# Kernel optimization log

Hardware: AMD Instinct MI355X
Metric: run time of the kernel (lower is better)

Reference implementation:

```python
import jax, jax.numpy as jnp
import numpy as np

B, IN, H, OUT = 4096, 1024, 2048, 1024
EPS = 1e-5  # added to std (not variance), matching the torch module


def _ln(z, a, b):
    # torch.std default is unbiased (ddof=1); eps added to sigma
    mu = jnp.mean(z, axis=1, keepdims=True)
    sigma = jnp.std(z, axis=1, ddof=1, keepdims=True)
    return (z - mu) / (sigma + EPS) * a + b


def setup_inputs() -> dict:
    key = jax.random.key(0)
    ks = iter(jax.random.split(key, 40))
    W = lambda i, o: (jax.random.normal(next(ks), (o, i), jnp.float32) / np.sqrt(i)).astype(jnp.float32)
    bz = lambda o: jnp.zeros((o,), jnp.float32)
    d = {
        "inp": jax.random.normal(next(ks), (B, IN), jnp.float32),
        "h_0": jax.random.normal(next(ks), (B, H), jnp.float32),
        "c_0": jax.random.normal(next(ks), (B, H), jnp.float32),
        # h-side gate linears (H -> H)
        "Wfh": W(H, H), "bfh": bz(H), "Wih": W(H, H), "bih": bz(H),
        "Wch": W(H, H), "bch": bz(H), "Woh": W(H, H), "boh": bz(H),
        # x-side gate linears (IN -> H)
        "Wfx": W(IN, H), "bfx": bz(H), "Wix": W(IN, H), "bix": bz(H),
        "Wcx": W(IN, H), "bcx": bz(H), "Wox": W(IN, H), "box": bz(H),
        # decoder (H -> OUT)
        "Wdec": W(H, OUT), "bdec": bz(OUT),
        # LayerNormalization params (a2 ones, b2 zeros), shape (1, H)
        "ax": jnp.ones((1, H), jnp.float32), "bx": jnp.zeros((1, H), jnp.float32),
        "ah": jnp.ones((1, H), jnp.float32), "bh": jnp.zeros((1, H), jnp.float32),
        "ac": jnp.ones((1, H), jnp.float32), "bc": jnp.zeros((1, H), jnp.float32),
    }
    return d


def reference(inp, h_0, c_0,
              Wfh, bfh, Wih, bih, Wch, bch, Woh, boh,
              Wfx, bfx, Wix, bix, Wcx, bcx, Wox, box,
              Wdec, bdec, ax, bx, ah, bh, ac, bc):
    lin = lambda x, W, b: x @ W.T + b
    gate = lambda wx, bx_, wh, bh_: (_ln(lin(inp, wx, bx_), ax, bx)
                                     + _ln(lin(h_0, wh, bh_), ah, bh))
    f_g = jax.nn.sigmoid(gate(Wfx, bfx, Wfh, bfh))
    i_g = jax.nn.sigmoid(gate(Wix, bix, Wih, bih))
    c_tilda = jnp.tanh(gate(Wcx, bcx, Wch, bch))
    cx = f_g * c_0 + i_g * c_tilda
    o_g = jax.nn.sigmoid(gate(Wox, box, Woh, boh))
    hx = o_g * jnp.tanh(_ln(cx, ac, bc))
    out = lin(hx, Wdec, bdec)  # decoder applied to hidden state (vectorized over batch)
    return (out, hx, cx)
```

## Files before the change

### kernel.cpp

```cpp
#include <hip/hip_runtime.h>

#define NB   4096
#define NIN  1024
#define NH   2048
#define NOUT 1024
#define NH4  8192

typedef short short8 __attribute__((ext_vector_type(8)));
typedef float f32x4 __attribute__((ext_vector_type(4)));
typedef float f32x16 __attribute__((ext_vector_type(16)));
typedef unsigned short ushort8v __attribute__((ext_vector_type(8)));

__device__ __forceinline__ float bf2f(unsigned short u) {
  union { unsigned int i; float f; } c; c.i = ((unsigned int)u) << 16; return c.f;
}
__device__ __forceinline__ unsigned short f2bf(float f) {
  union { float f; unsigned int i; } c; c.f = f;
  unsigned int u = c.i;
  u += 0x7FFFu + ((u >> 16) & 1u);
  return (unsigned short)(u >> 16);
}
__device__ __forceinline__ float sigf(float x) { return 1.0f / (1.0f + __expf(-x)); }
__device__ __forceinline__ float tanh_f(float x) { return 1.0f - 2.0f / (__expf(2.0f * x) + 1.0f); }

#define CNT_INP  ((size_t)NB * NIN)
#define CNT_H0   ((size_t)NB * NH)
#define CNT_WXG  ((size_t)NH * NIN)
#define CNT_WHG  ((size_t)NH * NH)
#define CNT_WD   ((size_t)NOUT * NH)
#define OFF_XB   ((size_t)0)
#define OFF_H0B  (OFF_XB + CNT_INP)
#define OFF_HXB  (OFF_H0B + CNT_H0)
#define OFF_WX   (OFF_HXB + CNT_H0)
#define OFF_WH   (OFF_WX + 4 * CNT_WXG)
#define OFF_WD   (OFF_WH + 4 * CNT_WHG)
#define OFF_ZX   (OFF_WD + CNT_WD)
#define OFF_ZH   (OFF_ZX + (size_t)NB * NH4)
#define CVT_TOTAL (OFF_WD + CNT_WD)

struct CvtArgs { const float* src[11]; };

__global__ __launch_bounds__(256) void cvt_all(CvtArgs a, unsigned short* __restrict__ dstBase) {
  const size_t i = ((size_t)blockIdx.x * 256 + threadIdx.x) * 8;
  if (i >= CVT_TOTAL) return;
  const size_t cnt[11] = {CNT_INP, CNT_H0, CNT_WXG, CNT_WXG, CNT_WXG, CNT_WXG,
                          CNT_WHG, CNT_WHG, CNT_WHG, CNT_WHG, CNT_WD};
  const size_t dst[11] = {OFF_XB, OFF_H0B,
                          OFF_WX, OFF_WX + CNT_WXG, OFF_WX + 2 * CNT_WXG, OFF_WX + 3 * CNT_WXG,
                          OFF_WH, OFF_WH + CNT_WHG, OFF_WH + 2 * CNT_WHG, OFF_WH + 3 * CNT_WHG,
                          OFF_WD};
  size_t base = 0;
#pragma unroll
  for (int s = 0; s < 11; s++) {
    if (i < base + cnt[s]) {
      const size_t off = i - base;
      const float* sp = a.src[s] + off;
      float4 v0 = *(const float4*)(sp);
      float4 v1 = *(const float4*)(sp + 4);
      ushort8v o;
      o[0] = f2bf(v0.x); o[1] = f2bf(v0.y); o[2] = f2bf(v0.z); o[3] = f2bf(v0.w);
      o[4] = f2bf(v1.x); o[5] = f2bf(v1.y); o[6] = f2bf(v1.z); o[7] = f2bf(v1.w);
      *(ushort8v*)(dstBase + dst[s] + off) = o;
      return;
    }
    base += cnt[s];
  }
}

__device__ __forceinline__ void gload16(const void* g, void* l) {
  __builtin_amdgcn_global_load_lds((const __attribute__((address_space(1))) void*)g,
                                   (__attribute__((address_space(3))) void*)l, 16, 0, 0);
}

#define SCH0  __builtin_amdgcn_sched_barrier(0)
#define BARR  __builtin_amdgcn_s_barrier()
#define LGKM0 asm volatile("s_waitcnt lgkmcnt(0)" ::: "memory")
#define VMC6  asm volatile("s_waitcnt vmcnt(6)" ::: "memory")
#define VMC0  asm volatile("s_waitcnt vmcnt(0)" ::: "memory")

__global__ __launch_bounds__(512) void gemm_dual8(
    const unsigned short* __restrict__ Xb, const unsigned short* __restrict__ Wx,
    const unsigned short* __restrict__ H0b, const unsigned short* __restrict__ Wh,
    const float* bx0, const float* bx1, const float* bx2, const float* bx3,
    const float* bh0, const float* bh1, const float* bh2, const float* bh3,
    unsigned short* __restrict__ Zx, unsigned short* __restrict__ Zh) {
  __shared__ __align__(16) unsigned short As[2][256 * 64];
  __shared__ __align__(16) unsigned short Bs[2][256 * 64];

  const unsigned short* Ag; const unsigned short* Bg;
  const float *p0, *p1, *p2, *p3; unsigned short* Cg; int K;
  if (blockIdx.z == 0) { Ag = Xb;  Bg = Wx; Cg = Zx; K = NIN; p0 = bx0; p1 = bx1; p2 = bx2; p3 = bx3; }
  else                 { Ag = H0b; Bg = Wh; Cg = Zh; K = NH;  p0 = bh0; p1 = bh1; p2 = bh2; p3 = bh3; }

  const int t    = threadIdx.x;
  const int wid  = t >> 6;
  const int lane = t & 63;
  const int m15  = lane & 15;
  const int g4   = lane >> 4;
  const int wm   = wid >> 2;
  const int wn   = wid & 3;
  const int rloc = lane >> 3;
  const int slot = lane & 7;
  const int ck   = slot ^ rloc ^ (wid & 3);
  const int m0   = blockIdx.y * 256;
  const int n0   = blockIdx.x * 256;
  const int NT   = K >> 6;
  const size_t thrOff = (size_t)(wid * 8 + rloc) * K + ck * 8;

#define STAGE_HALF(G, R0, H, TT, LDBASE) do {                                                     \
    const unsigned short* _gs = (G) + thrOff + (size_t)((R0) + (H) * 128) * K + (size_t)(TT) * 64; \
    unsigned short* _ld = (LDBASE) + ((H) * 128 + wid * 8) * 64;                                   \
    gload16(_gs, _ld);                                                                             \
    gload16(_gs + (size_t)64 * K, _ld + 4096);                                                     \
  } while (0)

#define LD8(S, ROW, KC) (*(const short8*)&(S)[(ROW) * 64 + (((KC) ^ (((ROW) & 7) ^ (((ROW) >> 3) & 3))) * 8)])

  f32x4 acc[8][4];
#pragma unroll
  for (int m = 0; m < 8; m++)
#pragma unroll
    for (int n = 0; n < 4; n++)
#pragma unroll
      for (int r = 0; r < 4; r++) acc[m][n][r] = 0.f;

  STAGE_HALF(Ag, m0, 0, 0, As[0]);
  STAGE_HALF(Ag, m0, 1, 0, As[0]);
  STAGE_HALF(Bg, n0, 0, 0, Bs[0]);
  STAGE_HALF(Bg, n0, 1, 0, Bs[0]);
  STAGE_HALF(Bg, n0, 0, 1, Bs[1]);
  STAGE_HALF(Bg, n0, 1, 1, Bs[1]);
  STAGE_HALF(Ag, m0, 0, 1, As[1]);
  VMC6;
  SCH0; BARR; SCH0;

  for (int kt = 0; kt < NT; ++kt) {
    const int cur = kt & 1;
    const unsigned short* sA = As[cur];
    const unsigned short* sB = Bs[cur];
    const int tp1 = (kt + 1 < NT) ? kt + 1 : NT - 1;
    const int tp2 = (kt + 2 < NT) ? kt + 2 : NT - 1;
    short8 b[4][2], a[4][2];

#pragma unroll
    for (int n = 0; n < 4; n++) {
      const int row = wn * 64 + n * 16 + m15;
      b[n][0] = LD8(sB, row, g4);
      b[n][1] = LD8(sB, row, 4 + g4);
    }
#pragma unroll
    for (int m = 0; m < 4; m++) {
      const int row = wm * 128 + m * 16 + m15;
      a[m][0] = LD8(sA, row, g4);
      a[m][1] = LD8(sA, row, 4 + g4);
    }
    STAGE_HALF(Ag, m0, 1, tp1, As[cur ^ 1]);
    SCH0; BARR; LGKM0; SCH0;
    __builtin_amdgcn_s_setprio(1);
#pragma unroll
    for (int m = 0; m < 4; m++)
#pragma unroll
      for (int n = 0; n < 2; n++) {
        acc[m][n] = __builtin_amdgcn_mfma_f32_16x16x32_bf16(a[m][0], b[n][0], acc[m][n], 0, 0, 0);
        acc[m][n] = __builtin_amdgcn_mfma_f32_16x16x32_bf16(a[m][1], b[n][1], acc[m][n], 0, 0, 0);
      }
    __builtin_amdgcn_s_setprio(0);
    SCH0; BARR; SCH0;

    STAGE_HALF(Bg, n0, 0, tp2, Bs[cur]);
    SCH0; BARR; LGKM0; SCH0;
    __builtin_amdgcn_s_setprio(1);
#pragma unroll
    for (int m = 0; m < 4; m++)
#pragma unroll
      for (int n = 0; n < 2; n++) {
        acc[m][2 + n] = __builtin_amdgcn_mfma_f32_16x16x32_bf16(a[m][0], b[2 + n][0], acc[m][2 + n], 0, 0, 0);
        acc[m][2 + n] = __builtin_amdgcn_mfma_f32_16x16x32_bf16(a[m][1], b[2 + n][1], acc[m][2 + n], 0, 0, 0);
      }
    __builtin_amdgcn_s_setprio(0);
    SCH0; BARR; SCH0;

#pragma unroll
    for (int m = 0; m < 4; m++) {
      const int row = wm * 128 + 64 + m * 16 + m15;
      a[m][0] = LD8(sA, row, g4);
      a[m][1] = LD8(sA, row, 4 + g4);
    }
    STAGE_HALF(Bg, n0, 1, tp2, Bs[cur]);
    SCH0; BARR; LGKM0; SCH0;
    __builtin_amdgcn_s_setprio(1);
#pragma unroll
    for (int m = 0; m < 4; m++)
#pragma unroll
      for (int n = 0; n < 2; n++) {
        acc[4 + m][n] = __builtin_amdgcn_mfma_f32_16x16x32_bf16(a[m][0], b[n][0], acc[4 + m][n], 0, 0, 0);
        acc[4 + m][n] = __builtin_amdgcn_mfma_f32_16x16x32_bf16(a[m][1], b[n][1], acc[4 + m][n], 0, 0, 0);
      }
    __builtin_amdgcn_s_setprio(0);
    SCH0; BARR; SCH0;

    STAGE_HALF(Ag, m0, 0, tp2, As[cur]);
    SCH0; BARR; SCH0;
    __builtin_amdgcn_s_setprio(1);
#pragma unroll
    for (int m = 0; m < 4; m++)
#pragma unroll
      for (int n = 0; n < 2; n++) {
        acc[4 + m][2 + n] = __builtin_amdgcn_mfma_f32_16x16x32_bf16(a[m][0], b[2 + n][0], acc[4 + m][2 + n], 0, 0, 0);
        acc[4 + m][2 + n] = __builtin_amdgcn_mfma_f32_16x16x32_bf16(a[m][1], b[2 + n][1], acc[4 + m][2 + n], 0, 0, 0);
      }
    __builtin_amdgcn_s_setprio(0);
    VMC6;
    SCH0; BARR; SCH0;
  }

  VMC0;

#pragma unroll
  for (int n = 0; n < 4; n++) {
    const int col = n0 + wn * 64 + n * 16 + m15;
    const float* bp = (col < 2048) ? p0 : ((col < 4096) ? p1 : ((col < 6144) ? p2 : p3));
    const float bv = bp[col & 2047];
#pragma unroll
    for (int m = 0; m < 8; m++) {
      const int rowb = m0 + wm * 128 + m * 16 + g4 * 4;
#pragma unroll
      for (int r = 0; r < 4; r++) {
        Cg[(size_t)(rowb + r) * NH4 + col] = f2bf(acc[m][n][r] + bv);
      }
    }
  }
#undef STAGE_HALF
#undef LD8
}

template<int MT, bool BOUT>
__device__ __forceinline__ void gemm_core32(const unsigned short* __restrict__ A,
                                            const unsigned short* __restrict__ Bm,
                                            const float* b0p, const float* b1p,
                                            const float* b2p, const float* b3p,
                                            float* __restrict__ Cf, unsigned short* __restrict__ Cb,
                                            int N, int K) {
  constexpr int TM = MT * 64;
  __shared__ __align__(16) unsigned short As[TM * 64];
  __shared__ __align__(16) unsigned short Bs[128 * 64];
  const int t = threadIdx.x;
  const int w = t >> 6;
  const int lane = t & 63;
  const int r31 = lane & 31;
  const int hi = lane >> 5;
  const int rloc = lane >> 3;
  const int slot = lane & 7;
  const int m0 = blockIdx.y * TM;
  const int n0 = blockIdx.x * 128;
  const int wm = (w >> 1) * (MT * 32);
  const int wn = (w & 1) * 64;

  f32x16 acc[MT][2];
#pragma unroll
  for (int i = 0; i < MT; i++)
#pragma unroll
    for (int j = 0; j < 2; j++)
#pragma unroll
      for (int r = 0; r < 16; r++) acc[i][j][r] = 0.f;

  const unsigned short* AgP[2 * MT];
  unsigned short* AsP[2 * MT];
#pragma unroll
  for (int q = 0; q < 2 * MT; q++) {
    const int iss = w + 4 * q;
    const int bblk = slot ^ rloc ^ (iss & 3);
    AgP[q] = A + (size_t)(m0 + iss * 8 + rloc) * K + bblk * 8;
    AsP[q] = As + iss * 512;
  }
  const unsigned short* BgP[4];
  unsigned short* BsP[4];
#pragma unroll
  for (int q = 0; q < 4; q++) {
    const int iss = w + 4 * q;
    const int bblk = slot ^ rloc ^ (iss & 3);
    BgP[q] = Bm + (size_t)(n0 + iss * 8 + rloc) * K + bblk * 8;
    BsP[q] = Bs + iss * 512;
  }

  const int swz = (r31 & 7) ^ ((r31 >> 3) & 3);

  for (int k0 = 0; k0 < K; k0 += 64) {
#pragma unroll
    for (int q = 0; q < 2 * MT; q++) gload16(AgP[q] + k0, AsP[q]);
#pragma unroll
    for (int q = 0; q < 4; q++) gload16(BgP[q] + k0, BsP[q]);
    __syncthreads();

#pragma unroll
    for (int ks = 0; ks < 4; ks++) {
      const int phys = ((ks * 2 + hi) ^ swz) * 8;
      short8 af[MT], bf[2];
#pragma unroll
      for (int mt = 0; mt < MT; mt++) af[mt] = *(const short8*)&As[(wm + mt * 32 + r31) * 64 + phys];
#pragma unroll
      for (int jt = 0; jt < 2; jt++) bf[jt] = *(const short8*)&Bs[(wn + jt * 32 + r31) * 64 + phys];
#pragma unroll
      for (int mt = 0; mt < MT; mt++)
#pragma unroll
        for (int jt = 0; jt < 2; jt++)
          acc[mt][jt] = __builtin_amdgcn_mfma_f32_32x32x16_bf16(af[mt], bf[jt], acc[mt][jt], 0, 0, 0);
    }
    __syncthreads();
  }

#pragma unroll
  for (int mt = 0; mt < MT; mt++) {
#pragma unroll
    for (int jt = 0; jt < 2; jt++) {
      const int col = n0 + wn + jt * 32 + r31;
      const float* bp = (col < 2048) ? b0p : ((col < 4096) ? b1p : ((col < 6144) ? b2p : b3p));
      const float bv = bp[col & 2047];
      const int rowb = m0 + wm + mt * 32 + hi * 4;
#pragma unroll
      for (int reg = 0; reg < 16; reg++) {
        const int row = rowb + (reg & 3) + 8 * (reg >> 2);
        const float v = acc[mt][jt][reg] + bv;
        const size_t idx = (size_t)row * N + col;
        if (BOUT) Cb[idx] = f2bf(v);
        else      Cf[idx] = v;
      }
    }
  }
}

__global__ __launch_bounds__(256) void gemm_dec(const unsigned short* __restrict__ HXb,
                                                const unsigned short* __restrict__ Wd,
                                                const float* __restrict__ bdec,
                                                float* __restrict__ out) {
  gemm_core32<1, false>(HXb, Wd, bdec, bdec, bdec, bdec, out, nullptr, NOUT, NH);
}

__global__ __launch_bounds__(256) void ln_gates(const unsigned short* __restrict__ Zx,
                                                const unsigned short* __restrict__ Zh,
                                                const float* __restrict__ c0,
                                                const float* __restrict__ ax, const float* __restrict__ bx,
                                                const float* __restrict__ ah, const float* __restrict__ bh,
                                                const float* __restrict__ ac, const float* __restrict__ bc,
                                                float* __restrict__ out_top,
                                                unsigned short* __restrict__ hx_bf) {
  const int b = blockIdx.x;
  const int t = threadIdx.x;
  const int n = t * 8;
  const int w = t >> 6;
  const int lane = t & 63;
  const float inv_n = 1.0f / 2048.0f, inv_nm1 = 1.0f / 2047.0f;

  short8 zx[4], zh[4];
  const size_t rowoff = (size_t)b * NH4;
#pragma unroll
  for (int g = 0; g < 4; g++) {
    zx[g] = *(const short8*)(Zx + rowoff + g * NH + n);
    zh[g] = *(const short8*)(Zh + rowoff + g * NH + n);
  }

  float s[16];
#pragma unroll
  for (int g = 0; g < 4; g++) {
    float su = 0, sq = 0, su2 = 0, sq2 = 0;
#pragma unroll
    for (int j = 0; j < 8; j++) {
      float v = bf2f((unsigned short)zx[g][j]); su += v; sq += v * v;
      float u = bf2f((unsigned short)zh[g][j]); su2 += u; sq2 += u * u;
    }
    s[g * 4 + 0] = su; s[g * 4 + 1] = sq; s[g * 4 + 2] = su2; s[g * 4 + 3] = sq2;
  }
#pragma unroll
  for (int i = 0; i < 16; i++) {
    float v = s[i];
#pragma unroll
    for (int o = 32; o > 0; o >>= 1) v += __shfl_xor(v, o, 64);
    s[i] = v;
  }
  __shared__ float red[4][16];
  __shared__ float red2[4][2];
  if (lane == 0) {
#pragma unroll
    for (int i = 0; i < 16; i++) red[w][i] = s[i];
  }
  __syncthreads();
#pragma unroll
  for (int i = 0; i < 16; i++) s[i] = red[0][i] + red[1][i] + red[2][i] + red[3][i];

  float mux[4], ivx[4], muh[4], ivh[4];
#pragma unroll
  for (int g = 0; g < 4; g++) {
    mux[g] = s[g * 4 + 0] * inv_n;
    float vx = fmaxf((s[g * 4 + 1] - s[g * 4 + 0] * mux[g]) * inv_nm1, 0.0f);
    ivx[g] = 1.0f / (sqrtf(vx) + 1e-5f);
    muh[g] = s[g * 4 + 2] * inv_n;
    float vh = fmaxf((s[g * 4 + 3] - s[g * 4 + 2] * muh[g]) * inv_nm1, 0.0f);
    ivh[g] = 1.0f / (sqrtf(vh) + 1e-5f);
  }

  float axl[8], bxl[8], ahl[8], bhl[8], c0l[8];
  *(float4*)&axl[0] = *(const float4*)(ax + n); *(float4*)&axl[4] = *(const float4*)(ax + n + 4);
  *(float4*)&bxl[0] = *(const float4*)(bx + n); *(float4*)&bxl[4] = *(const float4*)(bx + n + 4);
  *(float4*)&ahl[0] = *(const float4*)(ah + n); *(float4*)&ahl[4] = *(const float4*)(ah + n + 4);
  *(float4*)&bhl[0] = *(const float4*)(bh + n); *(float4*)&bhl[4] = *(const float4*)(bh + n + 4);
  const float* c0p = c0 + (size_t)b * NH + n;
  *(float4*)&c0l[0] = *(const float4*)(c0p); *(float4*)&c0l[4] = *(const float4*)(c0p + 4);

  float cx[8], og[8];
  float cs = 0, css = 0;
#pragma unroll
  for (int j = 0; j < 8; j++) {
    float pre[4];
#pragma unroll
    for (int g = 0; g < 4; g++) {
      float vx = bf2f((unsigned short)zx[g][j]);
      float vh = bf2f((unsigned short)zh[g][j]);
      pre[g] = ((vx - mux[g]) * ivx[g]) * axl[j] + bxl[j]
             + ((vh - muh[g]) * ivh[g]) * ahl[j] + bhl[j];
    }
    float fg = sigf(pre[0]);
    float ig = sigf(pre[1]);
    float ct = tanh_f(pre[2]);
    og[j] = sigf(pre[3]);
    float c = fg * c0l[j] + ig * ct;
    cx[j] = c; cs += c; css += c * c;
  }
#pragma unroll
  for (int o = 32; o > 0; o >>= 1) { cs += __shfl_xor(cs, o, 64); css += __shfl_xor(css, o, 64); }
  if (lane == 0) { red2[w][0] = cs; red2[w][1] = css; }
  __syncthreads();
  cs = red2[0][0] + red2[1][0] + red2[2][0] + red2[3][0];
  css = red2[0][1] + red2[1][1] + red2[2][1] + red2[3][1];
  const float muc = cs * inv_n;
  const float varc = fmaxf((css - cs * muc) * inv_nm1, 0.0f);
  const float ivc = 1.0f / (sqrtf(varc) + 1e-5f);

  float acl[8], bcl[8];
  *(float4*)&acl[0] = *(const float4*)(ac + n); *(float4*)&acl[4] = *(const float4*)(ac + n + 4);
  *(float4*)&bcl[0] = *(const float4*)(bc + n); *(float4*)&bcl[4] = *(const float4*)(bc + n + 4);

  float hx[8];
#pragma unroll
  for (int j = 0; j < 8; j++)
    hx[j] = og[j] * tanh_f((cx[j] - muc) * ivc * acl[j] + bcl[j]);

  float* hx_out = out_top + (size_t)NB * NOUT + (size_t)b * NH + n;
  float* cx_out = out_top + (size_t)NB * NOUT + (size_t)NB * NH + (size_t)b * NH + n;
  float4 v;
  v.x = hx[0]; v.y = hx[1]; v.z = hx[2]; v.w = hx[3]; *(float4*)(hx_out) = v;
  v.x = hx[4]; v.y = hx[5]; v.z = hx[6]; v.w = hx[7]; *(float4*)(hx_out + 4) = v;
  v.x = cx[0]; v.y = cx[1]; v.z = cx[2]; v.w = cx[3]; *(float4*)(cx_out) = v;
  v.x = cx[4]; v.y = cx[5]; v.z = cx[6]; v.w = cx[7]; *(float4*)(cx_out + 4) = v;
  ushort8v hb;
#pragma unroll
  for (int j = 0; j < 8; j++) hb[j] = f2bf(hx[j]);
  *(ushort8v*)(hx_bf + (size_t)b * NH + n) = hb;
}

extern "C" void kernel_launch(void* const* d_in, const int* in_sizes, int n_in,
                              void* d_out, int out_size, void* d_ws, size_t ws_size,
                              hipStream_t stream) {
  const float* inp = (const float*)d_in[0];
  const float* h0  = (const float*)d_in[1];
  const float* c0  = (const float*)d_in[2];
  const float* bhg[4] = {(const float*)d_in[4], (const float*)d_in[6], (const float*)d_in[8], (const float*)d_in[10]};
  const float* bxg[4] = {(const float*)d_in[12], (const float*)d_in[14], (const float*)d_in[16], (const float*)d_in[18]};
  const float* bdec = (const float*)d_in[20];
  const float* ax = (const float*)d_in[21];
  const float* bx = (const float*)d_in[22];
  const float* ah = (const float*)d_in[23];
  const float* bh = (const float*)d_in[24];
  const float* ac = (const float*)d_in[25];
  const float* bc = (const float*)d_in[26];

  unsigned short* wsb = (unsigned short*)d_ws;
  unsigned short* Xb   = wsb + OFF_XB;
  unsigned short* H0b  = wsb + OFF_H0B;
  unsigned short* HXb  = wsb + OFF_HXB;
  unsigned short* Wx4b = wsb + OFF_WX;
  unsigned short* Wh4b = wsb + OFF_WH;
  unsigned short* Wdb  = wsb + OFF_WD;
  unsigned short* Zx   = wsb + OFF_ZX;
  unsigned short* Zh   = wsb + OFF_ZH;

  CvtArgs ca;
  ca.src[0] = inp; ca.src[1] = h0;
  ca.src[2] = (const float*)d_in[11]; ca.src[3] = (const float*)d_in[13];
  ca.src[4] = (const float*)d_in[15]; ca.src[5] = (const float*)d_in[17];
  ca.src[6] = (const float*)d_in[3];  ca.src[7] = (const float*)d_in[5];
  ca.src[8] = (const float*)d_in[7];  ca.src[9] = (const float*)d_in[9];
  ca.src[10] = (const float*)d_in[19];
  {
    const size_t nthr = CVT_TOTAL / 8;
    cvt_all<<<dim3((unsigned)((nthr + 255) / 256)), dim3(256), 0, stream>>>(ca, wsb);
  }

  gemm_dual8<<<dim3(NH4 / 256, NB / 256, 2), 512, 0, stream>>>(
      Xb, Wx4b, H0b, Wh4b,
      bxg[0], bxg[1], bxg[2], bxg[3],
      bhg[0], bhg[1], bhg[2], bhg[3],
      Zx, Zh);

  ln_gates<<<dim3(NB), 256, 0, stream>>>(Zx, Zh, c0, ax, bx, ah, bh, ac, bc, (float*)d_out, HXb);

  gemm_dec<<<dim3(NOUT / 128, NB / 64), 256, 0, stream>>>(HXb, Wdb, bdec, (float*)d_out);
}
```

Baseline: 635.4 us.

## Rework LDS swizzle, split B fragment loads, and stage epilogue through LDS

Changes the LDS XOR swizzle to shift the row-group bits, which targets bank conflicts on the 16-byte fragment reads. B fragments are now loaded in two halves across phases, and the global prefetch stages for B are shifted later in the loop, which reschedules the prefetch overlap. The epilogue writes each bf16 16x64 tile into a padded per-wave LDS scratch and then issues 16-byte coalesced global stores, replacing the scattered 2-byte stores. This adds an extra barrier and LDS round trips, and it risks ordering hazards in the pipelined loads.

```diff
diff --git a/kernel.cpp b/kernel.cpp
--- a/kernel.cpp
+++ b/kernel.cpp
@@ -101,7 +101,7 @@
   const int wn   = wid & 3;
   const int rloc = lane >> 3;
   const int slot = lane & 7;
-  const int ck   = slot ^ rloc ^ (wid & 3);
+  const int ck   = slot ^ rloc ^ ((wid & 3) << 1);
   const int m0   = blockIdx.y * 256;
   const int n0   = blockIdx.x * 256;
   const int NT   = K >> 6;
@@ -114,7 +114,8 @@
     gload16(_gs + (size_t)64 * K, _ld + 4096);                                                     \
   } while (0)
 
-#define LD8(S, ROW, KC) (*(const short8*)&(S)[(ROW) * 64 + (((KC) ^ (((ROW) & 7) ^ (((ROW) >> 3) & 3))) * 8)])
+#define SWZ(R) (((R) & 7) ^ ((((R) >> 3) & 3) << 1))
+#define LD8(S, ROW, KC) (*(const short8*)&(S)[(ROW) * 64 + (((KC) ^ SWZ(ROW)) * 8)])
 
   f32x4 acc[8][4];
 #pragma unroll
@@ -143,7 +144,7 @@
     short8 b[4][2], a[4][2];
 
 #pragma unroll
-    for (int n = 0; n < 4; n++) {
+    for (int n = 0; n < 2; n++) {
       const int row = wn * 64 + n * 16 + m15;
       b[n][0] = LD8(sB, row, g4);
       b[n][1] = LD8(sB, row, 4 + g4);
@@ -167,7 +168,12 @@
     __builtin_amdgcn_s_setprio(0);
     SCH0; BARR; SCH0;
 
-    STAGE_HALF(Bg, n0, 0, tp2, Bs[cur]);
+#pragma unroll
+    for (int n = 2; n < 4; n++) {
+      const int row = wn * 64 + n * 16 + m15;
+      b[n][0] = LD8(sB, row, g4);
+      b[n][1] = LD8(sB, row, 4 + g4);
+    }
     SCH0; BARR; LGKM0; SCH0;
     __builtin_amdgcn_s_setprio(1);
 #pragma unroll
@@ -186,7 +192,7 @@
       a[m][0] = LD8(sA, row, g4);
       a[m][1] = LD8(sA, row, 4 + g4);
     }
-    STAGE_HALF(Bg, n0, 1, tp2, Bs[cur]);
+    STAGE_HALF(Bg, n0, 0, tp2, Bs[cur]);
     SCH0; BARR; LGKM0; SCH0;
     __builtin_amdgcn_s_setprio(1);
 #pragma unroll
@@ -199,6 +205,7 @@
     __builtin_amdgcn_s_setprio(0);
     SCH0; BARR; SCH0;
 
+    STAGE_HALF(Bg, n0, 1, tp2, Bs[cur]);
     STAGE_HALF(Ag, m0, 0, tp2, As[cur]);
     SCH0; BARR; SCH0;
     __builtin_amdgcn_s_setprio(1);
@@ -215,22 +222,38 @@
   }
 
   VMC0;
-
-#pragma unroll
-  for (int n = 0; n < 4; n++) {
-    const int col = n0 + wn * 64 + n * 16 + m15;
-    const float* bp = (col < 2048) ? p0 : ((col < 4096) ? p1 : ((col < 6144) ? p2 : p3));
-    const float bv = bp[col & 2047];
-#pragma unroll
-    for (int m = 0; m < 8; m++) {
-      const int rowb = m0 + wm * 128 + m * 16 + g4 * 4;
-#pragma unroll
-      for (int r = 0; r < 4; r++) {
-        Cg[(size_t)(rowb + r) * NH4 + col] = f2bf(acc[m][n][r] + bv);
+  SCH0; BARR; SCH0;
+
+  {
+    unsigned short* wls = &As[0][0] + wid * (16 * 68);
+    float bvn[4];
+#pragma unroll
+    for (int n = 0; n < 4; n++) {
+      const int col = n0 + wn * 64 + n * 16 + m15;
+      const float* bp = (col < 2048) ? p0 : ((col < 4096) ? p1 : ((col < 6144) ? p2 : p3));
+      bvn[n] = bp[col & 2047];
+    }
+    const int lrow0 = lane >> 3;
+    const int lcol0 = (lane & 7) * 8;
+#pragma unroll
+    for (int mt = 0; mt < 8; mt++) {
+#pragma unroll
+      for (int n = 0; n < 4; n++)
+#pragma unroll
+        for (int r = 0; r < 4; r++)
+          wls[(g4 * 4 + r) * 68 + n * 16 + m15] = f2bf(acc[mt][n][r] + bvn[n]);
+      LGKM0; SCH0;
+#pragma unroll
+      for (int i = 0; i < 2; i++) {
+        const int lrow = i * 8 + lrow0;
+        short8 v = *(const short8*)&wls[lrow * 68 + lcol0];
+        *(short8*)&Cg[(size_t)(m0 + wm * 128 + mt * 16 + lrow) * NH4 + (n0 + wn * 64 + lcol0)] = v;
       }
+      LGKM0; SCH0;
     }
   }
 #undef STAGE_HALF
+#undef SWZ
 #undef LD8
 }
 
```

New measurement: 578.6 us. 1.1x faster.
